# Performance work log

Hardware: AMD Instinct MI355X
Metric: run time of the kernel (lower is better)

## Reference

```python
import jax, jax.numpy as jnp
import numpy as np

N_SRC0, N_DST0, N_DST1 = 100000, 20000, 4000
E0, E1 = 640000, 128000
IN_F, HID_F, OUT_F = 512, 512, 256


def _graph_conv(x_src, src, dst, W, b, n_src, n_dst):
    """DGL GraphConv, norm='both': D_out^{-1/2} A D_in^{-1/2} X W + b."""
    ones_e = jnp.ones(src.shape[0], x_src.dtype)
    out_deg = jnp.maximum(jax.ops.segment_sum(ones_e, src, num_segments=n_src), 1.0)
    in_deg = jnp.maximum(jax.ops.segment_sum(ones_e, dst, num_segments=n_dst), 1.0)
    h = x_src * (out_deg ** -0.5)[:, None]          # [n_src, F] pre-normalize
    agg = jax.ops.segment_sum(h[src], dst, num_segments=n_dst)  # gather -> scatter-add
    agg = agg * (in_deg ** -0.5)[:, None]           # [n_dst, F]
    return agg @ W + b


def setup_inputs() -> dict:
    key = jax.random.key(0)
    ks = jax.random.split(key, 8)
    x = jax.random.normal(ks[0], (N_SRC0, IN_F), jnp.float32)
    src0 = jax.random.randint(ks[1], (E0,), 0, N_SRC0)
    dst0 = jax.random.randint(ks[2], (E0,), 0, N_DST0)
    src1 = jax.random.randint(ks[3], (E1,), 0, N_DST0)
    dst1 = jax.random.randint(ks[4], (E1,), 0, N_DST1)
    W1 = jax.random.normal(ks[5], (IN_F, HID_F), jnp.float32) * (IN_F ** -0.5)
    b1 = jnp.zeros((HID_F,), jnp.float32)
    W2 = jax.random.normal(ks[6], (HID_F, OUT_F), jnp.float32) * (HID_F ** -0.5)
    b2 = jnp.zeros((OUT_F,), jnp.float32)
    return {"x": x, "src0": src0, "dst0": dst0, "src1": src1, "dst1": dst1,
            "W1": W1, "b1": b1, "W2": W2, "b2": b2,
            "n_src0": N_SRC0, "n_dst0": N_DST0, "n_dst1": N_DST1}


def reference(x, src0, dst0, src1, dst1, W1, b1, W2, b2, n_src0, n_dst0, n_dst1):
    h = jax.nn.relu(_graph_conv(x, src0, dst0, W1, b1, n_src0, n_dst0))
    out = jax.nn.relu(_graph_conv(h, src1, dst1, W2, b2, n_dst0, n_dst1))
    return out
```

## Files before the change

kernel.cpp:

```cpp
#include <hip/hip_runtime.h>

typedef unsigned short ushort_t;
typedef unsigned int uint_t;
typedef __attribute__((ext_vector_type(8))) short s8v;
typedef __attribute__((ext_vector_type(4))) float f4v;

#define NS0 100000
#define ND0 20000
#define ND1 4000
#define E0  640000
#define E1  128000
#define F   512
#define OF  256
#define NCNT (NS0 + ND0 + ND0 + ND1)
#define SB  96

#define WBLK ((F * F + F * OF) / 256)

__device__ __forceinline__ ushort_t f2b(float f) {
    uint_t u = __float_as_uint(f);
    uint_t r = (u + 0x7fffu + ((u >> 16) & 1u)) >> 16;
    return (ushort_t)r;
}
__device__ __forceinline__ float b2f_lo(uint_t u) { return __uint_as_float(u << 16); }
__device__ __forceinline__ float b2f_hi(uint_t u) { return __uint_as_float(u & 0xffff0000u); }

__global__ __launch_bounds__(256) void prep(const int* __restrict__ src0, const int* __restrict__ dst0,
                                            const int* __restrict__ src1, const int* __restrict__ dst1,
                                            int* __restrict__ cntOut0, int* __restrict__ cntIn0,
                                            int* __restrict__ cntOut1, int* __restrict__ cntIn1,
                                            int* __restrict__ es0, int* __restrict__ es1,
                                            const float* __restrict__ W1, const float* __restrict__ W2,
                                            ushort_t* __restrict__ wt1, ushort_t* __restrict__ wt2) {
    int b = blockIdx.x;
    if (b < 625) {
        int e = (b * 256 + threadIdx.x) * 4;
        int4 s = *(const int4*)(src0 + e);
        int4 d = *(const int4*)(dst0 + e);
        atomicAdd(&cntOut0[s.x], 1);
        atomicAdd(&cntOut0[s.y], 1);
        atomicAdd(&cntOut0[s.z], 1);
        atomicAdd(&cntOut0[s.w], 1);
        int p0 = atomicAdd(&cntIn0[d.x], 1);
        int p1 = atomicAdd(&cntIn0[d.y], 1);
        int p2 = atomicAdd(&cntIn0[d.z], 1);
        int p3 = atomicAdd(&cntIn0[d.w], 1);
        es0[d.x * SB + min(p0, SB - 1)] = s.x;
        es0[d.y * SB + min(p1, SB - 1)] = s.y;
        es0[d.z * SB + min(p2, SB - 1)] = s.z;
        es0[d.w * SB + min(p3, SB - 1)] = s.w;
        return;
    }
    if (b < 750) {
        int e = ((b - 625) * 256 + threadIdx.x) * 4;
        int4 s = *(const int4*)(src1 + e);
        int4 d = *(const int4*)(dst1 + e);
        atomicAdd(&cntOut1[s.x], 1);
        atomicAdd(&cntOut1[s.y], 1);
        atomicAdd(&cntOut1[s.z], 1);
        atomicAdd(&cntOut1[s.w], 1);
        int p0 = atomicAdd(&cntIn1[d.x], 1);
        int p1 = atomicAdd(&cntIn1[d.y], 1);
        int p2 = atomicAdd(&cntIn1[d.z], 1);
        int p3 = atomicAdd(&cntIn1[d.w], 1);
        es1[d.x * SB + min(p0, SB - 1)] = s.x;
        es1[d.y * SB + min(p1, SB - 1)] = s.y;
        es1[d.z * SB + min(p2, SB - 1)] = s.z;
        es1[d.w * SB + min(p3, SB - 1)] = s.w;
        return;
    }
    int i = (b - 750) * 256 + threadIdx.x;
    if (i < F * F) {
        int k = i >> 9, n = i & (F - 1);
        wt1[n * F + k] = f2b(W1[i]);
    } else {
        int j = i - F * F;
        int k = j >> 8, n = j & (OF - 1);
        wt2[n * F + k] = f2b(W2[j]);
    }
}

__global__ __launch_bounds__(256) void gemm_xw(const float* __restrict__ A, const ushort_t* __restrict__ BT,
                                               const int* __restrict__ rowCnt, ushort_t* __restrict__ Y,
                                               int M, int K) {
    __shared__ __align__(16) ushort_t As[128 * 64];
    __shared__ __align__(16) ushort_t Bs[128 * 64];
    int tid = threadIdx.x;
    int lane = tid & 63, w = tid >> 6;
    int m16 = lane & 15, quad = lane >> 4;
    int wm = w & 1, wn = w >> 1;
    int bid = blockIdx.x;
    int wg = (bid & 7) * ((int)gridDim.x >> 3) + (bid >> 3);
    int nt = wg & 3, mt = wg >> 2;
    int bm = mt * 128, bn = nt * 128;
    const int N = 512;
    f4v acc[4][4] = {};
    for (int k0 = 0; k0 < K; k0 += 64) {
        f4v av[8];
        #pragma unroll
        for (int i = 0; i < 4; ++i) {
            int c = i * 256 + tid;
            int row = c >> 3, seg = (c & 7) * 8;
            int ra = bm + row; if (ra >= M) ra = M - 1;
            const f4v* srcp = (const f4v*)(A + (size_t)ra * K + k0 + seg);
            av[i * 2]     = __builtin_nontemporal_load(srcp);
            av[i * 2 + 1] = __builtin_nontemporal_load(srcp + 1);
        }
        #pragma unroll
        for (int i = 0; i < 4; ++i) {
            int c = i * 256 + tid;
            int row = c >> 3, seg = (c & 7) * 8;
            __builtin_amdgcn_global_load_lds(
                (const __attribute__((address_space(1))) uint_t*)(BT + (size_t)(bn + row) * K + k0 + seg),
                (__attribute__((address_space(3))) uint_t*)(Bs + (size_t)c * 8), 16, 0, 0);
        }
        #pragma unroll
        for (int i = 0; i < 4; ++i) {
            int c = i * 256 + tid;
            uint4 o;
            o.x = (uint_t)f2b(av[i * 2].x)     | ((uint_t)f2b(av[i * 2].y) << 16);
            o.y = (uint_t)f2b(av[i * 2].z)     | ((uint_t)f2b(av[i * 2].w) << 16);
            o.z = (uint_t)f2b(av[i * 2 + 1].x) | ((uint_t)f2b(av[i * 2 + 1].y) << 16);
            o.w = (uint_t)f2b(av[i * 2 + 1].z) | ((uint_t)f2b(av[i * 2 + 1].w) << 16);
            *(uint4*)(As + (size_t)c * 8) = o;
        }
        __syncthreads();
        #pragma unroll
        for (int kc = 0; kc < 2; ++kc) {
            int co = kc * 32 + quad * 8;
            s8v af[4], bf[4];
            #pragma unroll
            for (int m = 0; m < 4; ++m)
                af[m] = *(const s8v*)&As[(wm * 64 + m * 16 + m16) * 64 + co];
            #pragma unroll
            for (int nn = 0; nn < 4; ++nn)
                bf[nn] = *(const s8v*)&Bs[(wn * 64 + nn * 16 + m16) * 64 + co];
            #pragma unroll
            for (int m = 0; m < 4; ++m)
                #pragma unroll
                for (int nn = 0; nn < 4; ++nn)
                    acc[m][nn] = __builtin_amdgcn_mfma_f32_16x16x32_bf16(af[m], bf[nn], acc[m][nn], 0, 0, 0);
        }
        __syncthreads();
    }
    #pragma unroll
    for (int m = 0; m < 4; ++m) {
        #pragma unroll
        for (int rr = 0; rr < 4; ++rr) {
            int row = bm + wm * 64 + m * 16 + quad * 4 + rr;
            if (row < M) {
                float rs = rsqrtf(fmaxf((float)rowCnt[row], 1.0f));
                #pragma unroll
                for (int nn = 0; nn < 4; ++nn) {
                    int col = bn + wn * 64 + nn * 16 + m16;
                    Y[(size_t)row * N + col] = f2b(acc[m][nn][rr] * rs);
                }
            }
        }
    }
}

__device__ __forceinline__ void add8(float* acc, uint4 u) {
    acc[0] += b2f_lo(u.x); acc[1] += b2f_hi(u.x);
    acc[2] += b2f_lo(u.y); acc[3] += b2f_hi(u.y);
    acc[4] += b2f_lo(u.z); acc[5] += b2f_hi(u.z);
    acc[6] += b2f_lo(u.w); acc[7] += b2f_hi(u.w);
}

__global__ __launch_bounds__(256) void agg1(const ushort_t* __restrict__ Yb, const int* __restrict__ es,
                                            const int* __restrict__ cntIn, const int* __restrict__ cntOut1,
                                            const float* __restrict__ b1, ushort_t* __restrict__ out, int ndst) {
    int d = __builtin_amdgcn_readfirstlane(blockIdx.x * 4 + (threadIdx.x >> 6));
    if (d >= ndst) return;
    int lane = threadIdx.x & 63;
    int cntd = cntIn[d];
    int n = min(cntd, SB);
    const int* ed = es + (size_t)d * SB;
    const uint4* Xv = (const uint4*)Yb;
    float acc[8] = {0.f, 0.f, 0.f, 0.f, 0.f, 0.f, 0.f, 0.f};
    int c = n >> 3;
    int i = c << 3;
    if (c > 0) {
        int idP[8], idQ[8];
        uint4 uP[8], uQ[8];
        #pragma unroll
        for (int j = 0; j < 8; ++j) idP[j] = ed[j];
        #pragma unroll
        for (int j = 0; j < 8; ++j) uP[j] = Xv[(size_t)idP[j] * 64 + lane];
        if (c > 1) {
            #pragma unroll
            for (int j = 0; j < 8; ++j) idQ[j] = ed[8 + j];
        }
        int k = 0;
        while (true) {
            if (k + 1 < c) {
                #pragma unroll
                for (int j = 0; j < 8; ++j) uQ[j] = Xv[(size_t)idQ[j] * 64 + lane];
                if (k + 2 < c) {
                    #pragma unroll
                    for (int j = 0; j < 8; ++j) idP[j] = ed[(k + 2) * 8 + j];
                }
            }
            #pragma unroll
            for (int j = 0; j < 8; ++j) add8(acc, uP[j]);
            ++k;
            if (k >= c) break;
            if (k + 1 < c) {
                #pragma unroll
                for (int j = 0; j < 8; ++j) uP[j] = Xv[(size_t)idP[j] * 64 + lane];
                if (k + 2 < c) {
                    #pragma unroll
                    for (int j = 0; j < 8; ++j) idQ[j] = ed[(k + 2) * 8 + j];
                }
            }
            #pragma unroll
            for (int j = 0; j < 8; ++j) add8(acc, uQ[j]);
            ++k;
            if (k >= c) break;
        }
    }
    for (; i < n; ++i) add8(acc, Xv[(size_t)ed[i] * 64 + lane]);
    float rsIn = rsqrtf(fmaxf((float)cntd, 1.0f));
    float rsO1 = rsqrtf(fmaxf((float)cntOut1[d], 1.0f));
    const f4v* bb = (const f4v*)(b1 + lane * 8);
    f4v bA = bb[0], bB = bb[1];
    float v0 = fmaxf(acc[0] * rsIn + bA.x, 0.f) * rsO1;
    float v1 = fmaxf(acc[1] * rsIn + bA.y, 0.f) * rsO1;
    float v2 = fmaxf(acc[2] * rsIn + bA.z, 0.f) * rsO1;
    float v3 = fmaxf(acc[3] * rsIn + bA.w, 0.f) * rsO1;
    float v4 = fmaxf(acc[4] * rsIn + bB.x, 0.f) * rsO1;
    float v5 = fmaxf(acc[5] * rsIn + bB.y, 0.f) * rsO1;
    float v6 = fmaxf(acc[6] * rsIn + bB.z, 0.f) * rsO1;
    float v7 = fmaxf(acc[7] * rsIn + bB.w, 0.f) * rsO1;
    uint4 o;
    o.x = (uint_t)f2b(v0) | ((uint_t)f2b(v1) << 16);
    o.y = (uint_t)f2b(v2) | ((uint_t)f2b(v3) << 16);
    o.z = (uint_t)f2b(v4) | ((uint_t)f2b(v5) << 16);
    o.w = (uint_t)f2b(v6) | ((uint_t)f2b(v7) << 16);
    ((uint4*)out)[(size_t)d * 64 + lane] = o;
}

__global__ __launch_bounds__(256) void gemm_h2z(const ushort_t* __restrict__ A, const ushort_t* __restrict__ BT,
                                                ushort_t* __restrict__ C, int M, int N, int K) {
    __shared__ __align__(16) ushort_t As[128 * 64];
    __shared__ __align__(16) ushort_t Bs[128 * 64];
    int tid = threadIdx.x;
    int lane = tid & 63, w = tid >> 6;
    int m16 = lane & 15, quad = lane >> 4;
    int wm = w & 1, wn = w >> 1;
    int bm = blockIdx.x * 128, bn = blockIdx.y * 128;
    f4v acc[4][4] = {};
    for (int k0 = 0; k0 < K; k0 += 64) {
        #pragma unroll
        for (int i = 0; i < 4; ++i) {
            int c = i * 256 + tid;
            int row = c >> 3, seg = (c & 7) * 8;
            int ra = bm + row; if (ra >= M) ra = M - 1;
            __builtin_amdgcn_global_load_lds(
                (const __attribute__((address_space(1))) uint_t*)(A + (size_t)ra * K + k0 + seg),
                (__attribute__((address_space(3))) uint_t*)(As + (size_t)c * 8), 16, 0, 0);
        }
        #pragma unroll
        for (int i = 0; i < 4; ++i) {
            int c = i * 256 + tid;
            int row = c >> 3, seg = (c & 7) * 8;
            __builtin_amdgcn_global_load_lds(
                (const __attribute__((address_space(1))) uint_t*)(BT + (size_t)(bn + row) * K + k0 + seg),
                (__attribute__((address_space(3))) uint_t*)(Bs + (size_t)c * 8), 16, 0, 0);
        }
        __syncthreads();
        #pragma unroll
        for (int kc = 0; kc < 2; ++kc) {
            int co = kc * 32 + quad * 8;
            s8v af[4], bf[4];
            #pragma unroll
            for (int m = 0; m < 4; ++m)
                af[m] = *(const s8v*)&As[(wm * 64 + m * 16 + m16) * 64 + co];
            #pragma unroll
            for (int nn = 0; nn < 4; ++nn)
                bf[nn] = *(const s8v*)&Bs[(wn * 64 + nn * 16 + m16) * 64 + co];
            #pragma unroll
            for (int m = 0; m < 4; ++m)
                #pragma unroll
                for (int nn = 0; nn < 4; ++nn)
                    acc[m][nn] = __builtin_amdgcn_mfma_f32_16x16x32_bf16(af[m], bf[nn], acc[m][nn], 0, 0, 0);
        }
        __syncthreads();
    }
    #pragma unroll
    for (int m = 0; m < 4; ++m) {
        #pragma unroll
        for (int rr = 0; rr < 4; ++rr) {
            int row = bm + wm * 64 + m * 16 + quad * 4 + rr;
            if (row < M) {
                #pragma unroll
                for (int nn = 0; nn < 4; ++nn) {
                    int col = bn + wn * 64 + nn * 16 + m16;
                    C[(size_t)row * N + col] = f2b(acc[m][nn][rr]);
                }
            }
        }
    }
}

__global__ __launch_bounds__(256) void agg2(const ushort_t* __restrict__ Z, const int* __restrict__ es,
                                            const int* __restrict__ cntIn, const float* __restrict__ b2,
                                            float* __restrict__ out, int ndst) {
    int d = __builtin_amdgcn_readfirstlane(blockIdx.x * 4 + (threadIdx.x >> 6));
    if (d >= ndst) return;
    int lane = threadIdx.x & 63;
    int cntd = cntIn[d];
    int n = min(cntd, SB);
    const int* ed = es + (size_t)d * SB;
    const uint2* Zv = (const uint2*)Z;
    float a0 = 0.f, a1 = 0.f, a2 = 0.f, a3 = 0.f;
    int c = n >> 3;
    int i = c << 3;
    if (c > 0) {
        int idP[8], idQ[8];
        uint2 uP[8], uQ[8];
        #pragma unroll
        for (int j = 0; j < 8; ++j) idP[j] = ed[j];
        #pragma unroll
        for (int j = 0; j < 8; ++j) uP[j] = Zv[(size_t)idP[j] * 64 + lane];
        if (c > 1) {
            #pragma unroll
            for (int j = 0; j < 8; ++j) idQ[j] = ed[8 + j];
        }
        int k = 0;
        while (true) {
            if (k + 1 < c) {
                #pragma unroll
                for (int j = 0; j < 8; ++j) uQ[j] = Zv[(size_t)idQ[j] * 64 + lane];
                if (k + 2 < c) {
                    #pragma unroll
                    for (int j = 0; j < 8; ++j) idP[j] = ed[(k + 2) * 8 + j];
                }
            }
            #pragma unroll
            for (int j = 0; j < 8; ++j) {
                a0 += b2f_lo(uP[j].x); a1 += b2f_hi(uP[j].x);
                a2 += b2f_lo(uP[j].y); a3 += b2f_hi(uP[j].y);
            }
            ++k;
            if (k >= c) break;
            if (k + 1 < c) {
                #pragma unroll
                for (int j = 0; j < 8; ++j) uP[j] = Zv[(size_t)idP[j] * 64 + lane];
                if (k + 2 < c) {
                    #pragma unroll
                    for (int j = 0; j < 8; ++j) idQ[j] = ed[(k + 2) * 8 + j];
                }
            }
            #pragma unroll
            for (int j = 0; j < 8; ++j) {
                a0 += b2f_lo(uQ[j].x); a1 += b2f_hi(uQ[j].x);
                a2 += b2f_lo(uQ[j].y); a3 += b2f_hi(uQ[j].y);
            }
            ++k;
            if (k >= c) break;
        }
    }
    for (; i < n; ++i) {
        uint2 u = Zv[(size_t)ed[i] * 64 + lane];
        a0 += b2f_lo(u.x); a1 += b2f_hi(u.x);
        a2 += b2f_lo(u.y); a3 += b2f_hi(u.y);
    }
    float rs = rsqrtf(fmaxf((float)cntd, 1.0f));
    f4v bb = *(const f4v*)(b2 + lane * 4);
    f4v o;
    o.x = fmaxf(a0 * rs + bb.x, 0.f);
    o.y = fmaxf(a1 * rs + bb.y, 0.f);
    o.z = fmaxf(a2 * rs + bb.z, 0.f);
    o.w = fmaxf(a3 * rs + bb.w, 0.f);
    ((f4v*)out)[(size_t)d * 64 + lane] = o;
}

extern "C" void kernel_launch(void* const* d_in, const int* in_sizes, int n_in,
                              void* d_out, int out_size, void* d_ws, size_t ws_size,
                              hipStream_t stream) {
    (void)in_sizes; (void)n_in; (void)out_size; (void)ws_size;
    const float* x    = (const float*)d_in[0];
    const int*   src0 = (const int*)d_in[1];
    const int*   dst0 = (const int*)d_in[2];
    const int*   src1 = (const int*)d_in[3];
    const int*   dst1 = (const int*)d_in[4];
    const float* W1   = (const float*)d_in[5];
    const float* b1   = (const float*)d_in[6];
    const float* W2   = (const float*)d_in[7];
    const float* b2   = (const float*)d_in[8];
    float* out = (float*)d_out;

    char* p = (char*)d_ws;
    auto alloc = [&](size_t bytes) { char* q = p; p += (bytes + 255) & ~(size_t)255; return q; };
    int*      cnt  = (int*)alloc((size_t)NCNT * 4);
    int*      es0  = (int*)alloc((size_t)ND0 * SB * 4);
    int*      es1  = (int*)alloc((size_t)ND1 * SB * 4);
    ushort_t* wt1  = (ushort_t*)alloc((size_t)F * F * 2);
    ushort_t* wt2  = (ushort_t*)alloc((size_t)OF * F * 2);
    ushort_t* y    = (ushort_t*)alloc((size_t)NS0 * F * 2);
    ushort_t* hp   = (ushort_t*)alloc((size_t)ND0 * F * 2);
    ushort_t* z    = (ushort_t*)alloc((size_t)ND0 * OF * 2);

    int* cntOut0 = cnt;
    int* cntIn0  = cnt + NS0;
    int* cntOut1 = cnt + NS0 + ND0;
    int* cntIn1  = cnt + NS0 + ND0 + ND0;

    (void)hipMemsetAsync(cnt, 0, (size_t)NCNT * 4, stream);

    prep<<<750 + WBLK, 256, 0, stream>>>(src0, dst0, src1, dst1,
                                         cntOut0, cntIn0, cntOut1, cntIn1, es0, es1,
                                         W1, W2, wt1, wt2);

    gemm_xw<<<3128, 256, 0, stream>>>(x, wt1, cntOut0, y, NS0, F);

    agg1<<<(ND0 + 3) / 4, 256, 0, stream>>>(y, es0, cntIn0, cntOut1, b1, hp, ND0);

    gemm_h2z<<<dim3((ND0 + 127) / 128, OF / 128), 256, 0, stream>>>(hp, wt2, z, ND0, OF, F);

    agg2<<<(ND1 + 3) / 4, 256, 0, stream>>>(z, es1, cntIn1, b2, out, ND1);
}
```

Measured before the change: 613.9 us.

## Load A fragments directly into registers and double-buffer B tiles in GEMMs

Both GEMMs are merged into one templated kernel. A fragments now go from global memory straight into MFMA registers, with no LDS staging, and fp32 inputs are converted with a hardware packed bf16 convert instruction. B tiles are double-buffered in LDS so the load of the next k-step overlaps the current MFMAs. The block-to-tile remap now accounts for XCD interleaving with uneven counts. Each wave re-reads A rows from global memory without sharing them across wn waves, which doubles A global traffic. The convert instruction may also round differently from the software f2b.

```diff
diff --git a/kernel.cpp b/kernel.cpp
--- a/kernel.cpp
+++ b/kernel.cpp
@@ -24,6 +24,12 @@
 }
 __device__ __forceinline__ float b2f_lo(uint_t u) { return __uint_as_float(u << 16); }
 __device__ __forceinline__ float b2f_hi(uint_t u) { return __uint_as_float(u & 0xffff0000u); }
+__device__ __forceinline__ uint_t cvtpk(float lo, float hi) {
+    uint_t r;
+    asm("v_cvt_pk_bf16_f32 %0, %1, %2" : "=v"(r) : "v"(lo), "v"(hi));
+    return r;
+}
+typedef union { s8v v; uint4 u; } s8u;
 
 __global__ __launch_bounds__(256) void prep(const int* __restrict__ src0, const int* __restrict__ dst0,
                                             const int* __restrict__ src1, const int* __restrict__ dst1,
@@ -80,68 +86,97 @@
     }
 }
 
-__global__ __launch_bounds__(256) void gemm_xw(const float* __restrict__ A, const ushort_t* __restrict__ BT,
-                                               const int* __restrict__ rowCnt, ushort_t* __restrict__ Y,
-                                               int M, int K) {
-    __shared__ __align__(16) ushort_t As[128 * 64];
-    __shared__ __align__(16) ushort_t Bs[128 * 64];
+template <bool AF32>
+__global__ __launch_bounds__(256) void gemmA(const void* __restrict__ Ap, const ushort_t* __restrict__ BT,
+                                             const int* __restrict__ rowCnt, ushort_t* __restrict__ Y,
+                                             int M, int N, int K) {
+    __shared__ __align__(16) ushort_t Bs[2 * 128 * 64];
     int tid = threadIdx.x;
     int lane = tid & 63, w = tid >> 6;
     int m16 = lane & 15, quad = lane >> 4;
     int wm = w & 1, wn = w >> 1;
-    int bid = blockIdx.x;
-    int wg = (bid & 7) * ((int)gridDim.x >> 3) + (bid >> 3);
-    int nt = wg & 3, mt = wg >> 2;
+    int nwg = (int)gridDim.x;
+    int q = nwg >> 3, r = nwg & 7;
+    int xcd = (int)blockIdx.x & 7, jj = (int)blockIdx.x >> 3;
+    int wg = (xcd < r ? xcd * (q + 1) : r * (q + 1) + (xcd - r) * q) + jj;
+    int ntiles = N >> 7;
+    int nt = wg % ntiles, mt = wg / ntiles;
     int bm = mt * 128, bn = nt * 128;
-    const int N = 512;
     f4v acc[4][4] = {};
-    for (int k0 = 0; k0 < K; k0 += 64) {
-        f4v av[8];
-        #pragma unroll
-        for (int i = 0; i < 4; ++i) {
-            int c = i * 256 + tid;
-            int row = c >> 3, seg = (c & 7) * 8;
-            int ra = bm + row; if (ra >= M) ra = M - 1;
-            const f4v* srcp = (const f4v*)(A + (size_t)ra * K + k0 + seg);
-            av[i * 2]     = __builtin_nontemporal_load(srcp);
-            av[i * 2 + 1] = __builtin_nontemporal_load(srcp + 1);
-        }
-        #pragma unroll
-        for (int i = 0; i < 4; ++i) {
-            int c = i * 256 + tid;
-            int row = c >> 3, seg = (c & 7) * 8;
+
+    auto stage = [&](int t, int buf) {
+        #pragma unroll
+        for (int i2 = 0; i2 < 4; ++i2) {
+            int c2 = i2 * 256 + tid;
+            int row = c2 >> 3, seg = (c2 & 7) * 8;
             __builtin_amdgcn_global_load_lds(
-                (const __attribute__((address_space(1))) uint_t*)(BT + (size_t)(bn + row) * K + k0 + seg),
-                (__attribute__((address_space(3))) uint_t*)(Bs + (size_t)c * 8), 16, 0, 0);
-        }
-        #pragma unroll
-        for (int i = 0; i < 4; ++i) {
-            int c = i * 256 + tid;
-            uint4 o;
-            o.x = (uint_t)f2b(av[i * 2].x)     | ((uint_t)f2b(av[i * 2].y) << 16);
-            o.y = (uint_t)f2b(av[i * 2].z)     | ((uint_t)f2b(av[i * 2].w) << 16);
-            o.z = (uint_t)f2b(av[i * 2 + 1].x) | ((uint_t)f2b(av[i * 2 + 1].y) << 16);
-            o.w = (uint_t)f2b(av[i * 2 + 1].z) | ((uint_t)f2b(av[i * 2 + 1].w) << 16);
-            *(uint4*)(As + (size_t)c * 8) = o;
-        }
-        __syncthreads();
+                (const __attribute__((address_space(1))) uint_t*)(BT + (size_t)(bn + row) * K + t * 64 + seg),
+                (__attribute__((address_space(3))) uint_t*)(Bs + buf * 8192 + (size_t)c2 * 8), 16, 0, 0);
+        }
+    };
+
+    int nk = K >> 6;
+    int cur = 0;
+    stage(0, 0);
+    __syncthreads();
+    for (int t = 0; t < nk; ++t) {
+        if (t + 1 < nk) stage(t + 1, cur ^ 1);
+        int k0 = t * 64;
+        const ushort_t* bsc = Bs + cur * 8192;
+        s8v af0[4], af1[4];
+        if constexpr (AF32) {
+            const float* A = (const float*)Ap;
+            f4v aL0[4], aH0[4], aL1[4], aH1[4];
+            #pragma unroll
+            for (int m = 0; m < 4; ++m) {
+                int ra = bm + wm * 64 + m * 16 + m16; if (ra >= M) ra = M - 1;
+                const f4v* ap = (const f4v*)(A + (size_t)ra * K + k0 + quad * 8);
+                aL0[m] = __builtin_nontemporal_load(ap);
+                aH0[m] = __builtin_nontemporal_load(ap + 1);
+                aL1[m] = __builtin_nontemporal_load(ap + 8);
+                aH1[m] = __builtin_nontemporal_load(ap + 9);
+            }
+            #pragma unroll
+            for (int m = 0; m < 4; ++m) {
+                s8u t0, t1;
+                t0.u.x = cvtpk(aL0[m].x, aL0[m].y);
+                t0.u.y = cvtpk(aL0[m].z, aL0[m].w);
+                t0.u.z = cvtpk(aH0[m].x, aH0[m].y);
+                t0.u.w = cvtpk(aH0[m].z, aH0[m].w);
+                af0[m] = t0.v;
+                t1.u.x = cvtpk(aL1[m].x, aL1[m].y);
+                t1.u.y = cvtpk(aL1[m].z, aL1[m].w);
+                t1.u.z = cvtpk(aH1[m].x, aH1[m].y);
+                t1.u.w = cvtpk(aH1[m].z, aH1[m].w);
+                af1[m] = t1.v;
+            }
+        } else {
+            const ushort_t* A = (const ushort_t*)Ap;
+            #pragma unroll
+            for (int m = 0; m < 4; ++m) {
+                int ra = bm + wm * 64 + m * 16 + m16; if (ra >= M) ra = M - 1;
+                const ushort_t* ap = A + (size_t)ra * K + k0 + quad * 8;
+                af0[m] = *(const s8v*)ap;
+                af1[m] = *(const s8v*)(ap + 32);
+            }
+        }
         #pragma unroll
         for (int kc = 0; kc < 2; ++kc) {
             int co = kc * 32 + quad * 8;
-            s8v af[4], bf[4];
-            #pragma unroll
-            for (int m = 0; m < 4; ++m)
-                af[m] = *(const s8v*)&As[(wm * 64 + m * 16 + m16) * 64 + co];
+            s8v bf[4];
             #pragma unroll
             for (int nn = 0; nn < 4; ++nn)
-                bf[nn] = *(const s8v*)&Bs[(wn * 64 + nn * 16 + m16) * 64 + co];
-            #pragma unroll
-            for (int m = 0; m < 4; ++m)
+                bf[nn] = *(const s8v*)&bsc[(wn * 64 + nn * 16 + m16) * 64 + co];
+            #pragma unroll
+            for (int m = 0; m < 4; ++m) {
+                s8v a = (kc == 0) ? af0[m] : af1[m];
                 #pragma unroll
                 for (int nn = 0; nn < 4; ++nn)
-                    acc[m][nn] = __builtin_amdgcn_mfma_f32_16x16x32_bf16(af[m], bf[nn], acc[m][nn], 0, 0, 0);
+                    acc[m][nn] = __builtin_amdgcn_mfma_f32_16x16x32_bf16(a, bf[nn], acc[m][nn], 0, 0, 0);
+            }
         }
         __syncthreads();
+        cur ^= 1;
     }
     #pragma unroll
     for (int m = 0; m < 4; ++m) {
@@ -149,7 +184,7 @@
         for (int rr = 0; rr < 4; ++rr) {
             int row = bm + wm * 64 + m * 16 + quad * 4 + rr;
             if (row < M) {
-                float rs = rsqrtf(fmaxf((float)rowCnt[row], 1.0f));
+                float rs = rowCnt ? rsqrtf(fmaxf((float)rowCnt[row], 1.0f)) : 1.0f;
                 #pragma unroll
                 for (int nn = 0; nn < 4; ++nn) {
                     int col = bn + wn * 64 + nn * 16 + m16;
@@ -240,69 +275,6 @@
     ((uint4*)out)[(size_t)d * 64 + lane] = o;
 }
 
-__global__ __launch_bounds__(256) void gemm_h2z(const ushort_t* __restrict__ A, const ushort_t* __restrict__ BT,
-                                                ushort_t* __restrict__ C, int M, int N, int K) {
-    __shared__ __align__(16) ushort_t As[128 * 64];
-    __shared__ __align__(16) ushort_t Bs[128 * 64];
-    int tid = threadIdx.x;
-    int lane = tid & 63, w = tid >> 6;
-    int m16 = lane & 15, quad = lane >> 4;
-    int wm = w & 1, wn = w >> 1;
-    int bm = blockIdx.x * 128, bn = blockIdx.y * 128;
-    f4v acc[4][4] = {};
-    for (int k0 = 0; k0 < K; k0 += 64) {
-        #pragma unroll
-        for (int i = 0; i < 4; ++i) {
-            int c = i * 256 + tid;
-            int row = c >> 3, seg = (c & 7) * 8;
-            int ra = bm + row; if (ra >= M) ra = M - 1;
-            __builtin_amdgcn_global_load_lds(
-                (const __attribute__((address_space(1))) uint_t*)(A + (size_t)ra * K + k0 + seg),
-                (__attribute__((address_space(3))) uint_t*)(As + (size_t)c * 8), 16, 0, 0);
-        }
-        #pragma unroll
-        for (int i = 0; i < 4; ++i) {
-            int c = i * 256 + tid;
-            int row = c >> 3, seg = (c & 7) * 8;
-            __builtin_amdgcn_global_load_lds(
-                (const __attribute__((address_space(1))) uint_t*)(BT + (size_t)(bn + row) * K + k0 + seg),
-                (__attribute__((address_space(3))) uint_t*)(Bs + (size_t)c * 8), 16, 0, 0);
-        }
-        __syncthreads();
-        #pragma unroll
-        for (int kc = 0; kc < 2; ++kc) {
-            int co = kc * 32 + quad * 8;
-            s8v af[4], bf[4];
-            #pragma unroll
-            for (int m = 0; m < 4; ++m)
-                af[m] = *(const s8v*)&As[(wm * 64 + m * 16 + m16) * 64 + co];
-            #pragma unroll
-            for (int nn = 0; nn < 4; ++nn)
-                bf[nn] = *(const s8v*)&Bs[(wn * 64 + nn * 16 + m16) * 64 + co];
-            #pragma unroll
-            for (int m = 0; m < 4; ++m)
-                #pragma unroll
-                for (int nn = 0; nn < 4; ++nn)
-                    acc[m][nn] = __builtin_amdgcn_mfma_f32_16x16x32_bf16(af[m], bf[nn], acc[m][nn], 0, 0, 0);
-        }
-        __syncthreads();
-    }
-    #pragma unroll
-    for (int m = 0; m < 4; ++m) {
-        #pragma unroll
-        for (int rr = 0; rr < 4; ++rr) {
-            int row = bm + wm * 64 + m * 16 + quad * 4 + rr;
-            if (row < M) {
-                #pragma unroll
-                for (int nn = 0; nn < 4; ++nn) {
-                    int col = bn + wn * 64 + nn * 16 + m16;
-                    C[(size_t)row * N + col] = f2b(acc[m][nn][rr]);
-                }
-            }
-        }
-    }
-}
-
 __global__ __launch_bounds__(256) void agg2(const ushort_t* __restrict__ Z, const int* __restrict__ es,
                                             const int* __restrict__ cntIn, const float* __restrict__ b2,
                                             float* __restrict__ out, int ndst) {
@@ -413,11 +385,11 @@
                                          cntOut0, cntIn0, cntOut1, cntIn1, es0, es1,
                                          W1, W2, wt1, wt2);
 
-    gemm_xw<<<3128, 256, 0, stream>>>(x, wt1, cntOut0, y, NS0, F);
+    gemmA<true><<<3128, 256, 0, stream>>>(x, wt1, cntOut0, y, NS0, F, F);
 
     agg1<<<(ND0 + 3) / 4, 256, 0, stream>>>(y, es0, cntIn0, cntOut1, b1, hp, ND0);
 
-    gemm_h2z<<<dim3((ND0 + 127) / 128, OF / 128), 256, 0, stream>>>(hp, wt2, z, ND0, OF, F);
+    gemmA<false><<<314, 256, 0, stream>>>(hp, wt2, nullptr, z, ND0, OF, F);
 
     agg2<<<(ND1 + 3) / 4, 256, 0, stream>>>(z, es1, cntIn1, b2, out, ND1);
 }
```

Measured after the change: 725.2 us. 18.1% more time.
